# Optimization experiments

Hardware: AMD Instinct MI355X
Metric: run time of the kernel (lower is better)

The kernel has to match this reference:

```python
import jax, jax.numpy as jnp
import numpy as np

N_NODES, N_EDGES, N_FEAT, N_HID = 50000, 800000, 512, 64


def gcn_conv(x, W, b, src, dst, ew):
    """PyG-style GCNConv: linear -> symmetric-normalized aggregation with self-loops -> +bias."""
    N = x.shape[0]
    h = x @ W  # [N, H]
    # degree includes the implicit self-loop of weight 1 (PyG gcn_norm default)
    deg = jax.ops.segment_sum(ew, dst, num_segments=N) + 1.0
    dinv = jax.lax.rsqrt(deg)  # deg^{-1/2}
    coef = dinv[src] * ew * dinv[dst]  # [E]
    out = jax.ops.segment_sum(h[src] * coef[:, None], dst, num_segments=N)
    out = out + h * (dinv * dinv)[:, None]  # self-loop contribution
    return out + b


def setup_inputs() -> dict:
    key = jax.random.key(0)
    k0, k1, k2, k3 = jax.random.split(key, 4)
    x = jax.random.normal(k0, (N_NODES, N_FEAT), dtype=jnp.float32)
    edge_index = jax.random.randint(k1, (2, N_EDGES), 0, N_NODES, dtype=jnp.int64)
    edge_weight = jnp.ones((N_EDGES,), dtype=jnp.float32)
    W1 = jax.random.normal(k2, (N_FEAT, N_HID), dtype=jnp.float32) * (1.0 / np.sqrt(N_FEAT))
    b1 = jnp.zeros((N_HID,), dtype=jnp.float32)
    W2 = jax.random.normal(k3, (N_HID, N_HID), dtype=jnp.float32) * (1.0 / np.sqrt(N_HID))
    b2 = jnp.zeros((N_HID,), dtype=jnp.float32)
    return {"x": x, "edge_index": edge_index, "edge_weight": edge_weight,
            "W1": W1, "b1": b1, "W2": W2, "b2": b2}


def reference(x, edge_index, edge_weight, W1, b1, W2, b2):
    # Grace.forward -> GCN_body.forward in eval mode (no dropout, no LN)
    src, dst = edge_index[0], edge_index[1]
    h = jax.nn.relu(gcn_conv(x, W1, b1, src, dst, edge_weight))
    h = jax.nn.relu(gcn_conv(h, W2, b2, src, dst, edge_weight))
    return h
```

## Files before the change

kernel.cpp:

```cpp
#include <hip/hip_runtime.h>
#include <hip/hip_bf16.h>

typedef __bf16 bf16x8 __attribute__((ext_vector_type(8)));
typedef float  f32x4  __attribute__((ext_vector_type(4)));

#define RNODES 64
#define ROWCAP 1792
#define NB 256
#define MAXNR 1024
#define FIXB 256

__device__ __forceinline__ float bf_lo(unsigned int v) { return __uint_as_float(v << 16); }
__device__ __forceinline__ float bf_hi(unsigned int v) { return __uint_as_float(v & 0xFFFF0000u); }

__device__ __forceinline__ void pack_one(const void* __restrict__ W, int f16,
                                         __hip_bfloat16* __restrict__ Wp, int K, int t) {
    int j  = t & 7;
    int l  = (t >> 3) & 63;
    int nt = (t >> 9) & 3;
    int kt = t >> 11;
    int k = kt * 32 + (l >> 4) * 8 + j;
    int n = nt * 16 + (l & 15);
    size_t gi = (size_t)k * 64 + n;
    Wp[t] = f16 ? ((const __hip_bfloat16*)W)[gi]
                : __float2bfloat16(((const float*)W)[gi]);
}

__global__ void setup_kernel(const unsigned int* __restrict__ ew_raw,
                             const unsigned int* __restrict__ ei_raw,
                             const void* __restrict__ W1, const void* __restrict__ W2,
                             int* __restrict__ flags,
                             __hip_bfloat16* __restrict__ W1p, __hip_bfloat16* __restrict__ W2p,
                             int F, int H) {
    int f16 = (ew_raw[0] == 0x3F803F80u) ? 1 : 0;
    if (blockIdx.x == 0 && threadIdx.x == 0) {
        flags[0] = f16;
        flags[1] = ((ei_raw[1] | ei_raw[3] | ei_raw[5] | ei_raw[7]) == 0u) ? 1 : 0;
        flags[2] = 0;
        flags[3] = 0;
        flags[4] = 1;
    }
    int t = blockIdx.x * 256 + threadIdx.x;
    if (t < F * 64)            pack_one(W1, f16, W1p, F, t);
    else if (t < (F + H) * 64) pack_one(W2, f16, W2p, H, t - F * 64);
}

__device__ __forceinline__ void gemm_body(const void* __restrict__ A,
                                          const __hip_bfloat16* __restrict__ Wp,
                                          int a_f32, __hip_bfloat16* __restrict__ out,
                                          int M, int K, int gt) {
    int wid  = gt >> 6;
    int lane = gt & 63;
    if (wid >= (M >> 4)) return;
    int row0 = wid << 4;
    int quad = lane >> 4, mr = lane & 15;

    const bf16x8* bp = (const bf16x8*)((const void*)Wp) + lane;

    f32x4 acc[4];
    #pragma unroll
    for (int nt = 0; nt < 4; ++nt) acc[nt] = (f32x4){0.f, 0.f, 0.f, 0.f};

    int KT = K >> 5;
    const __hip_bfloat16* ab   = (const __hip_bfloat16*)A + (size_t)(row0 + mr) * K + quad * 8;
    const float*          af32 = (const float*)A + (size_t)(row0 + mr) * K + quad * 8;

    int kt = 0;
    for (; kt + 4 <= KT; kt += 4) {
        bf16x8 af[4];
        if (a_f32) {
            #pragma unroll
            for (int u = 0; u < 4; ++u) {
                const float* ar = af32 + (kt + u) * 32;
                #pragma unroll
                for (int j = 0; j < 8; ++j) af[u][j] = (__bf16)ar[j];
            }
        } else {
            #pragma unroll
            for (int u = 0; u < 4; ++u)
                af[u] = ((const bf16x8*)((const void*)(ab + (kt + u) * 32)))[0];
        }
        #pragma unroll
        for (int u = 0; u < 4; ++u)
            #pragma unroll
            for (int nt = 0; nt < 4; ++nt) {
                bf16x8 bf = bp[((kt + u) * 4 + nt) * 64];
                acc[nt] = __builtin_amdgcn_mfma_f32_16x16x32_bf16(af[u], bf, acc[nt], 0, 0, 0);
            }
    }
    for (; kt < KT; ++kt) {
        bf16x8 af;
        if (a_f32) {
            const float* ar = af32 + kt * 32;
            #pragma unroll
            for (int j = 0; j < 8; ++j) af[j] = (__bf16)ar[j];
        } else {
            af = ((const bf16x8*)((const void*)(ab + kt * 32)))[0];
        }
        #pragma unroll
        for (int nt = 0; nt < 4; ++nt) {
            bf16x8 bf = bp[(kt * 4 + nt) * 64];
            acc[nt] = __builtin_amdgcn_mfma_f32_16x16x32_bf16(af, bf, acc[nt], 0, 0, 0);
        }
    }

    __hip_bfloat16* o = out + (size_t)row0 * 64;
    #pragma unroll
    for (int nt = 0; nt < 4; ++nt)
        #pragma unroll
        for (int r = 0; r < 4; ++r)
            o[(size_t)(quad * 4 + r) * 64 + nt * 16 + mr] = __float2bfloat16(acc[nt][r]);
}

__global__ void gemm_mfma(const void* __restrict__ A, const __hip_bfloat16* __restrict__ Wp,
                          const int* __restrict__ flags, __hip_bfloat16* __restrict__ out,
                          int M, int K, int a_mode) {
    int gt = blockIdx.x * blockDim.x + threadIdx.x;
    int a_f32 = (a_mode == 2) && (flags[0] == 0);
    gemm_body(A, Wp, a_f32, out, M, K, gt);
}

__global__ void bgp1_kernel(const void* __restrict__ A, const __hip_bfloat16* __restrict__ Wp,
                            __hip_bfloat16* __restrict__ outH,
                            const int* __restrict__ ei, const void* __restrict__ ew,
                            int* __restrict__ flags,
                            int* __restrict__ blockhist, unsigned int* __restrict__ pkstage,
                            int M, int K, int E, int NR, int gblocks) {
    if ((int)blockIdx.x < gblocks) {
        int gt = blockIdx.x * 256 + threadIdx.x;
        gemm_body(A, Wp, flags[0] == 0, outH, M, K, gt);
        return;
    }
    __shared__ int hist[MAXNR];
    int b = blockIdx.x - gblocks, tid = threadIdx.x;
    for (int i = tid; i < NR; i += 256) hist[i] = 0;
    __syncthreads();
    int f16 = flags[0], i64 = flags[1];

    int nw = f16 ? (E >> 1) : E;
    unsigned int expect = f16 ? 0x3F803F80u : 0x3F800000u;
    int wchunk = (nw + NB - 1) / NB;
    int w0 = b * wchunk, w1 = w0 + wchunk; if (w1 > nw) w1 = nw;
    const unsigned int* ewr = (const unsigned int*)ew;
    unsigned int bad = 0;
    for (int i = w0 + tid; i < w1; i += 256) bad |= (ewr[i] ^ expect);
    if (bad) flags[4] = 0;

    int chunk = (E + NB - 1) / NB;
    int e0 = b * chunk, e1 = e0 + chunk; if (e1 > E) e1 = E;
    for (int e = e0 + tid; e < e1; e += 256) {
        int s, d;
        if (i64) { s = ei[2LL * e]; d = ei[2LL * ((long long)E + e)]; }
        else     { s = ei[e];       d = ei[E + e]; }
        int r = d >> 6;
        atomicAdd(&hist[r], 1);
        pkstage[e] = ((unsigned int)r << 22) | ((unsigned int)s << 6) | (unsigned int)(d & 63);
    }
    __syncthreads();
    for (int i = tid; i < NR; i += 256) blockhist[b * NR + i] = hist[i];
}

__device__ __forceinline__ void check_body(const void* __restrict__ A, const void* __restrict__ W,
                                           int* __restrict__ flags,
                                           const __hip_bfloat16* __restrict__ out,
                                           int N, int K, int a_mode, int fidx, int bid) {
    __shared__ float xs[4 * 512];
    int f16 = flags[0];
    int a_f32 = (a_mode == 2) && (f16 == 0);
    int tid = threadIdx.x;
    int total = 4 * K;
    for (int t = tid; t < total; t += 256) {
        int nn = t / K, kk = t - nn * K;
        int n = (int)(((long long)(bid * 4 + nn) * 977) % N);
        long long gi = (long long)n * K + kk;
        float v = a_f32 ? (float)(__bf16)(((const float*)A)[gi])
                        : __bfloat162float(((const __hip_bfloat16*)A)[gi]);
        xs[t] = v;
    }
    __syncthreads();
    int j = tid & 63, local = tid >> 6;
    int n = (int)(((long long)(bid * 4 + local) * 977) % N);
    const float* xr = xs + local * K;
    float acc = 0.f;
    if (f16) {
        const __hip_bfloat16* Wb = (const __hip_bfloat16*)W;
        #pragma unroll 8
        for (int k = 0; k < K; ++k) acc += xr[k] * __bfloat162float(Wb[(long long)k * 64 + j]);
    } else {
        const float* Wf = (const float*)W;
        #pragma unroll 8
        for (int k = 0; k < K; ++k) acc += xr[k] * (float)(__bf16)(Wf[(long long)k * 64 + j]);
    }
    float d = __bfloat162float(out[(size_t)n * 64 + j]) - acc;
    if (!(fabsf(d) <= 0.05f)) atomicAdd(&flags[fidx], 1);
}

__device__ __forceinline__ void fix_body(const void* __restrict__ A, const void* __restrict__ W,
                                         const int* __restrict__ flags,
                                         __hip_bfloat16* __restrict__ out,
                                         int N, int K, int a_mode, int fidx,
                                         int bid, int nblocks) {
    if (flags[fidx] == 0) return;
    __shared__ float xs[4 * 512];
    int tid = threadIdx.x;
    int f16 = flags[0];
    int a_f32 = (a_mode == 2) && (f16 == 0);
    int total = 4 * K;
    for (int node0 = bid * 4; node0 < N; node0 += nblocks * 4) {
        __syncthreads();
        for (int t = tid; t < total; t += 256) {
            int nn = t / K, kk = t - nn * K;
            if (node0 + nn < N) {
                long long gi = (long long)(node0 + nn) * K + kk;
                xs[t] = a_f32 ? ((const float*)A)[gi]
                              : __bfloat162float(((const __hip_bfloat16*)A)[gi]);
            }
        }
        __syncthreads();
        int j = tid & 63, local = tid >> 6;
        int n = node0 + local;
        if (n < N) {
            const float* xr = xs + local * K;
            float acc = 0.f;
            if (f16) {
                const __hip_bfloat16* Wb = (const __hip_bfloat16*)W;
                #pragma unroll 8
                for (int k = 0; k < K; ++k) acc += xr[k] * __bfloat162float(Wb[(long long)k * 64 + j]);
            } else {
                const float* Wf = (const float*)W;
                #pragma unroll 8
                for (int k = 0; k < K; ++k) acc += xr[k] * Wf[(long long)k * 64 + j];
            }
            out[(long long)n * 64 + j] = __float2bfloat16(acc);
        }
    }
}

__global__ void p2chk_kernel(int* __restrict__ blockhist, int* __restrict__ rtot, int NR,
                             const void* __restrict__ A, const void* __restrict__ W,
                             int* __restrict__ flags, const __hip_bfloat16* __restrict__ out,
                             int N, int K, int a_mode, int fidx, int p2b) {
    if ((int)blockIdx.x < p2b) {
        int r = blockIdx.x * 256 + threadIdx.x;
        if (r >= NR) return;
        int run = r * ROWCAP;
        #pragma unroll 4
        for (int b = 0; b < NB; ++b) {
            int c = blockhist[b * NR + r];
            blockhist[b * NR + r] = run;
            run += c;
        }
        int tot = run - r * ROWCAP;
        rtot[r] = tot > ROWCAP ? ROWCAP : tot;
    } else {
        check_body(A, W, flags, out, N, K, a_mode, fidx, blockIdx.x - p2b);
    }
}

__global__ void p3fix_kernel(const int* __restrict__ blockhist,
                             const unsigned int* __restrict__ pkstage,
                             const void* __restrict__ ew, const int* __restrict__ flags,
                             unsigned int* __restrict__ sortedR, float* __restrict__ sortedRW,
                             int E, int NR,
                             const void* __restrict__ A, const void* __restrict__ W,
                             __hip_bfloat16* __restrict__ out,
                             int N, int K, int a_mode, int fidx) {
    if ((int)blockIdx.x < NB) {
        __shared__ int loff[MAXNR];
        int b = blockIdx.x, tid = threadIdx.x;
        for (int i = tid; i < NR; i += 256) loff[i] = blockhist[b * NR + i];
        __syncthreads();
        int chunk = (E + NB - 1) / NB;
        int e0 = b * chunk, e1 = e0 + chunk; if (e1 > E) e1 = E;
        int ones = flags[4], f16 = flags[0];
        for (int e = e0 + tid; e < e1; e += 256) {
            unsigned int pk = pkstage[e];
            int r = (int)(pk >> 22);
            int pos = atomicAdd(&loff[r], 1);
            if (pos < (r + 1) * ROWCAP) {
                sortedR[pos] = pk;
                if (!ones) {
                    float w = f16 ? __bfloat162float(((const __hip_bfloat16*)ew)[e])
                                  : ((const float*)ew)[e];
                    sortedRW[pos] = w;
                }
            }
        }
    } else {
        fix_body(A, W, flags, out, N, K, a_mode, fidx, blockIdx.x - NB, FIXB);
    }
}

__global__ void range_kernel(const unsigned int* __restrict__ sortedR,
                             const float* __restrict__ sortedRW,
                             const int* __restrict__ rtot, const int* __restrict__ flags,
                             int* __restrict__ cnt, float* __restrict__ dinv,
                             int* __restrict__ row_ptr,
                             int* __restrict__ sortedS, float* __restrict__ sortedW, int N) {
    __shared__ unsigned int sd[ROWCAP];
    __shared__ float sw[ROWCAP];
    __shared__ int   cnt0[RNODES], pref[RNODES], slot[RNODES];
    __shared__ float wsum[RNODES];

    int r   = blockIdx.x;
    int tid = threadIdx.x;
    int ones = flags[4];
    int T = rtot[r];

    if (tid < RNODES) { cnt0[tid] = 0; wsum[tid] = 0.f; }
    __syncthreads();

    size_t g = (size_t)r * ROWCAP;
    for (int t = tid; t < T; t += 256) {
        sd[t] = sortedR[g + t];
        if (!ones) sw[t] = sortedRW[g + t];
    }
    __syncthreads();

    for (int k = tid; k < T; k += 256) {
        int dl = sd[k] & (RNODES - 1);
        atomicAdd(&cnt0[dl], 1);
        if (!ones) atomicAdd(&wsum[dl], sw[k]);
    }
    __syncthreads();

    if (tid < RNODES) pref[tid] = cnt0[tid];
    __syncthreads();
    for (int off = 1; off < RNODES; off <<= 1) {
        int v = (tid < RNODES && tid >= off) ? pref[tid - off] : 0;
        __syncthreads();
        if (tid < RNODES) pref[tid] += v;
        __syncthreads();
    }
    if (tid < RNODES) {
        int excl = pref[tid] - cnt0[tid];
        int n = r * RNODES + tid;
        slot[tid] = r * ROWCAP + excl;
        if (n < N) {
            cnt[n]     = cnt0[tid];
            row_ptr[n] = r * ROWCAP + excl;
            float wd = ones ? (float)cnt0[tid] : wsum[tid];
            dinv[n]  = rsqrtf(wd + 1.0f);
        }
    }
    __syncthreads();

    for (int k = tid; k < T; k += 256) {
        unsigned int v = sd[k];
        int dl = v & (RNODES - 1);
        int p = atomicAdd(&slot[dl], 1);
        sortedS[p] = (int)((v >> 6) & 0xFFFFu);
        if (!ones) sortedW[p] = sw[k];
    }
}

__global__ void check_fast(const void* __restrict__ A, const void* __restrict__ W,
                           int* __restrict__ flags, const __hip_bfloat16* __restrict__ out,
                           int N, int K, int a_mode, int fidx) {
    check_body(A, W, flags, out, N, K, a_mode, fidx, blockIdx.x);
}

__global__ void gemm_fix(const void* __restrict__ A, const void* __restrict__ W,
                         const int* __restrict__ flags, __hip_bfloat16* __restrict__ out,
                         int N, int K, int a_mode, int fidx) {
    fix_body(A, W, flags, out, N, K, a_mode, fidx, blockIdx.x, FIXB);
}

__global__ void gather_kernel(const __hip_bfloat16* __restrict__ h,
                              const int* __restrict__ sortedS, const float* __restrict__ sortedW,
                              const int* __restrict__ cnt, const int* __restrict__ row_ptr,
                              const float* __restrict__ dinv,
                              const void* __restrict__ bias, const int* __restrict__ flags,
                              void* __restrict__ out, int internal, int N) {
    int gt = blockIdx.x * blockDim.x + threadIdx.x;
    int n = gt >> 5, jl = gt & 31;
    if (n >= N) return;
    int f16 = flags[0], ones = flags[4];
    float dn = dinv[n];
    int deg = cnt[n];
    int base = row_ptr[n];
    const int*   p  = sortedS + base;
    const float* pw = sortedW + base;
    const unsigned int* h32 = (const unsigned int*)h;
    float a0 = 0.f, a1 = 0.f;
    int s = 0;
    for (; s + 4 <= deg; s += 4) {
        int s0 = p[s], s1 = p[s + 1], s2 = p[s + 2], s3 = p[s + 3];
        float c0 = dinv[s0] * dn, c1 = dinv[s1] * dn;
        float c2 = dinv[s2] * dn, c3 = dinv[s3] * dn;
        if (!ones) { c0 *= pw[s]; c1 *= pw[s + 1]; c2 *= pw[s + 2]; c3 *= pw[s + 3]; }
        unsigned int v0 = h32[(size_t)s0 * 32 + jl];
        unsigned int v1 = h32[(size_t)s1 * 32 + jl];
        unsigned int v2 = h32[(size_t)s2 * 32 + jl];
        unsigned int v3 = h32[(size_t)s3 * 32 + jl];
        a0 += c0 * bf_lo(v0) + c1 * bf_lo(v1) + c2 * bf_lo(v2) + c3 * bf_lo(v3);
        a1 += c0 * bf_hi(v0) + c1 * bf_hi(v1) + c2 * bf_hi(v2) + c3 * bf_hi(v3);
    }
    for (; s < deg; ++s) {
        int s0 = p[s];
        float c = dinv[s0] * dn;
        if (!ones) c *= pw[s];
        unsigned int v = h32[(size_t)s0 * 32 + jl];
        a0 += c * bf_lo(v);
        a1 += c * bf_hi(v);
    }
    unsigned int vs = h32[(size_t)n * 32 + jl];
    float dn2 = dn * dn;
    a0 += dn2 * bf_lo(vs);
    a1 += dn2 * bf_hi(vs);
    if (f16) {
        unsigned int bv = ((const unsigned int*)bias)[jl];
        a0 += bf_lo(bv);
        a1 += bf_hi(bv);
    } else {
        a0 += ((const float*)bias)[jl * 2];
        a1 += ((const float*)bias)[jl * 2 + 1];
    }
    a0 = fmaxf(a0, 0.f);
    a1 = fmaxf(a1, 0.f);
    if (internal | f16) {
        __hip_bfloat16 b0 = __float2bfloat16(a0), b1 = __float2bfloat16(a1);
        unsigned int pack = ((unsigned int)(*(unsigned short*)&b1) << 16)
                          | (unsigned int)(*(unsigned short*)&b0);
        ((unsigned int*)out)[(size_t)n * 32 + jl] = pack;
    } else {
        ((float*)out)[(size_t)n * 64 + jl * 2]     = a0;
        ((float*)out)[(size_t)n * 64 + jl * 2 + 1] = a1;
    }
}

extern "C" void kernel_launch(void* const* d_in, const int* in_sizes, int n_in,
                              void* d_out, int out_size, void* d_ws, size_t ws_size,
                              hipStream_t stream) {
    const void* x  = d_in[0];
    const int*  ei = (const int*)d_in[1];
    const void* ew = d_in[2];
    const void* W1 = d_in[3];
    const void* b1 = d_in[4];
    const void* W2 = d_in[5];
    const void* b2 = d_in[6];

    const int H = in_sizes[4];
    const int F = in_sizes[3] / H;
    const int N = in_sizes[0] / F;
    const int E = in_sizes[1] / 2;

    const int NR = (N + RNODES - 1) / RNODES;

    char* w = (char*)d_ws;
    size_t off = 0;
    auto alloc = [&](size_t bytes) {
        char* r = w + off;
        off += (bytes + 255) & ~(size_t)255;
        return r;
    };
    int*   flags     = (int*)alloc(32);
    int*   blockhist = (int*)alloc((size_t)NB * NR * 4);
    int*   rtot      = (int*)alloc((size_t)NR * 4);
    int*   cnt       = (int*)alloc((size_t)N * 4);
    float* dinv      = (float*)alloc((size_t)N * 4);
    int*   row_ptr   = (int*)alloc((size_t)N * 4);
    unsigned int* pkstage = (unsigned int*)alloc((size_t)E * 4);
    unsigned int* sortedR = (unsigned int*)alloc((size_t)NR * ROWCAP * 4);
    float* sortedRW  = (float*)alloc((size_t)NR * ROWCAP * 4);
    int*   sortedS   = (int*)alloc((size_t)NR * ROWCAP * 4);
    float* sortedW   = (float*)alloc((size_t)NR * ROWCAP * 4);
    __hip_bfloat16* bufH = (__hip_bfloat16*)alloc((size_t)N * 64 * 2);
    __hip_bfloat16* bufR = (__hip_bfloat16*)alloc((size_t)N * 64 * 2);
    __hip_bfloat16* W1p  = (__hip_bfloat16*)alloc((size_t)F * 64 * 2);
    __hip_bfloat16* W2p  = (__hip_bfloat16*)alloc((size_t)H * 64 * 2);

    int gblocks = ((N / 16) * 64 + 255) / 256;
    int p2b = (NR + 255) / 256;

    setup_kernel<<<((F + H) * 64 + 255) / 256, 256, 0, stream>>>(
        (const unsigned int*)ew, (const unsigned int*)ei, W1, W2, flags, W1p, W2p, F, H);

    bgp1_kernel<<<gblocks + NB, 256, 0, stream>>>(x, W1p, bufH, ei, ew, flags,
                                                  blockhist, pkstage,
                                                  N, F, E, NR, gblocks);

    p2chk_kernel<<<p2b + 64, 256, 0, stream>>>(blockhist, rtot, NR,
                                               x, W1, flags, bufH, N, F, 2, 2, p2b);

    p3fix_kernel<<<NB + FIXB, 256, 0, stream>>>(blockhist, pkstage, ew, flags,
                                                sortedR, sortedRW, E, NR,
                                                x, W1, bufH, N, F, 2, 2);

    range_kernel<<<NR, 256, 0, stream>>>(sortedR, sortedRW, rtot, flags,
                                         cnt, dinv, row_ptr, sortedS, sortedW, N);

    gather_kernel<<<(N * 32 + 255) / 256, 256, 0, stream>>>(bufH, sortedS, sortedW,
                                                            cnt, row_ptr, dinv,
                                                            b1, flags, bufR, 1, N);
    gemm_mfma<<<gblocks, 256, 0, stream>>>(bufR, W2p, flags, bufH, N, H, 0);
    check_fast<<<64, 256, 0, stream>>>(bufR, W2, flags, bufH, N, H, 0, 3);
    gemm_fix<<<FIXB, 256, 0, stream>>>(bufR, W2, flags, bufH, N, H, 0, 3);

    gather_kernel<<<(N * 32 + 255) / 256, 256, 0, stream>>>(bufH, sortedS, sortedW,
                                                            cnt, row_ptr, dinv,
                                                            b2, flags, d_out, 0, N);
}
```

Baseline: 313.3 us.

## Halve histogram blocks, wave-parallel prefix scan, deeper GEMM K unroll

Cuts the number of edge-bucketing blocks from 256 to 128, which halves the per-row histogram scan length. The scan over those blocks becomes wave-parallel, with one 64-lane wavefront per row using shuffle-up instead of a serial loop per thread. The MFMA GEMM inner loop is unrolled over 8 K-tiles instead of 4 to issue more loads before the MFMAs. Fewer binning blocks means less parallelism in the histogram and scatter phases, and the deeper unroll raises register pressure.

```diff
diff --git a/kernel.cpp b/kernel.cpp
--- a/kernel.cpp
+++ b/kernel.cpp
@@ -6,7 +6,7 @@
 
 #define RNODES 64
 #define ROWCAP 1792
-#define NB 256
+#define NB 128
 #define MAXNR 1024
 #define FIXB 256
 
@@ -54,7 +54,6 @@
     if (wid >= (M >> 4)) return;
     int row0 = wid << 4;
     int quad = lane >> 4, mr = lane & 15;
-
     const bf16x8* bp = (const bf16x8*)((const void*)Wp) + lane;
 
     f32x4 acc[4];
@@ -62,54 +61,52 @@
     for (int nt = 0; nt < 4; ++nt) acc[nt] = (f32x4){0.f, 0.f, 0.f, 0.f};
 
     int KT = K >> 5;
-    const __hip_bfloat16* ab   = (const __hip_bfloat16*)A + (size_t)(row0 + mr) * K + quad * 8;
-    const float*          af32 = (const float*)A + (size_t)(row0 + mr) * K + quad * 8;
+    const __hip_bfloat16* ab    = (const __hip_bfloat16*)A + (size_t)(row0 + mr) * K + quad * 8;
+    const float*          af32p = (const float*)A + (size_t)(row0 + mr) * K + quad * 8;
 
     int kt = 0;
-    for (; kt + 4 <= KT; kt += 4) {
-        bf16x8 af[4];
+    for (; kt + 8 <= KT; kt += 8) {
+        bf16x8 af[8];
         if (a_f32) {
             #pragma unroll
-            for (int u = 0; u < 4; ++u) {
-                const float* ar = af32 + (kt + u) * 32;
+            for (int u = 0; u < 8; ++u) {
+                const float* ar = af32p + (kt + u) * 32;
                 #pragma unroll
                 for (int j = 0; j < 8; ++j) af[u][j] = (__bf16)ar[j];
             }
         } else {
             #pragma unroll
-            for (int u = 0; u < 4; ++u)
+            for (int u = 0; u < 8; ++u)
                 af[u] = ((const bf16x8*)((const void*)(ab + (kt + u) * 32)))[0];
         }
         #pragma unroll
-        for (int u = 0; u < 4; ++u)
+        for (int u = 0; u < 8; ++u)
             #pragma unroll
-            for (int nt = 0; nt < 4; ++nt) {
-                bf16x8 bf = bp[((kt + u) * 4 + nt) * 64];
-                acc[nt] = __builtin_amdgcn_mfma_f32_16x16x32_bf16(af[u], bf, acc[nt], 0, 0, 0);
-            }
+            for (int nt = 0; nt < 4; ++nt)
+                acc[nt] = __builtin_amdgcn_mfma_f32_16x16x32_bf16(
+                              af[u], bp[((kt + u) * 4 + nt) * 64], acc[nt], 0, 0, 0);
     }
     for (; kt < KT; ++kt) {
         bf16x8 af;
         if (a_f32) {
-            const float* ar = af32 + kt * 32;
+            const float* ar = af32p + kt * 32;
             #pragma unroll
             for (int j = 0; j < 8; ++j) af[j] = (__bf16)ar[j];
         } else {
             af = ((const bf16x8*)((const void*)(ab + kt * 32)))[0];
         }
         #pragma unroll
-        for (int nt = 0; nt < 4; ++nt) {
-            bf16x8 bf = bp[(kt * 4 + nt) * 64];
-            acc[nt] = __builtin_amdgcn_mfma_f32_16x16x32_bf16(af, bf, acc[nt], 0, 0, 0);
-        }
+        for (int nt = 0; nt < 4; ++nt)
+            acc[nt] = __builtin_amdgcn_mfma_f32_16x16x32_bf16(
+                          af, bp[(kt * 4 + nt) * 64], acc[nt], 0, 0, 0);
     }
 
     __hip_bfloat16* o = out + (size_t)row0 * 64;
     #pragma unroll
     for (int nt = 0; nt < 4; ++nt)
         #pragma unroll
-        for (int r = 0; r < 4; ++r)
-            o[(size_t)(quad * 4 + r) * 64 + nt * 16 + mr] = __float2bfloat16(acc[nt][r]);
+        for (int rr = 0; rr < 4; ++rr)
+            o[(size_t)(quad * 4 + rr) * 64 + nt * 16 + mr] = __float2bfloat16(acc[nt][rr]);
 }
 
 __global__ void gemm_mfma(const void* __restrict__ A, const __hip_bfloat16* __restrict__ Wp,
@@ -127,8 +124,7 @@
                             int* __restrict__ blockhist, unsigned int* __restrict__ pkstage,
                             int M, int K, int E, int NR, int gblocks) {
     if ((int)blockIdx.x < gblocks) {
-        int gt = blockIdx.x * 256 + threadIdx.x;
-        gemm_body(A, Wp, flags[0] == 0, outH, M, K, gt);
+        gemm_body(A, Wp, flags[0] == 0, outH, M, K, blockIdx.x * 256 + threadIdx.x);
         return;
     }
     __shared__ int hist[MAXNR];
@@ -241,17 +237,24 @@
                              int* __restrict__ flags, const __hip_bfloat16* __restrict__ out,
                              int N, int K, int a_mode, int fidx, int p2b) {
     if ((int)blockIdx.x < p2b) {
-        int r = blockIdx.x * 256 + threadIdx.x;
-        if (r >= NR) return;
-        int run = r * ROWCAP;
-        #pragma unroll 4
-        for (int b = 0; b < NB; ++b) {
-            int c = blockhist[b * NR + r];
-            blockhist[b * NR + r] = run;
-            run += c;
-        }
-        int tot = run - r * ROWCAP;
-        rtot[r] = tot > ROWCAP ? ROWCAP : tot;
+        int r    = blockIdx.x * 4 + (threadIdx.x >> 6);
+        int lane = threadIdx.x & 63;
+        if (r < NR) {
+            int b0 = lane * 2;
+            int c0 = blockhist[(size_t)b0 * NR + r];
+            int c1 = blockhist[(size_t)(b0 + 1) * NR + r];
+            int s = c0 + c1;
+            int incl = s;
+            #pragma unroll
+            for (int off = 1; off < 64; off <<= 1) {
+                int t = __shfl_up(incl, off, 64);
+                if (lane >= off) incl += t;
+            }
+            int run = r * ROWCAP + (incl - s);
+            blockhist[(size_t)b0 * NR + r]       = run;
+            blockhist[(size_t)(b0 + 1) * NR + r] = run + c0;
+            if (lane == 63) rtot[r] = incl > ROWCAP ? ROWCAP : incl;
+        }
     } else {
         check_body(A, W, flags, out, N, K, a_mode, fidx, blockIdx.x - p2b);
     }
@@ -471,7 +474,7 @@
     __hip_bfloat16* W2p  = (__hip_bfloat16*)alloc((size_t)H * 64 * 2);
 
     int gblocks = ((N / 16) * 64 + 255) / 256;
-    int p2b = (NR + 255) / 256;
+    int p2b = (NR + 3) / 4;
 
     setup_kernel<<<((F + H) * 64 + 255) / 256, 256, 0, stream>>>(
         (const unsigned int*)ew, (const unsigned int*)ei, W1, W2, flags, W1p, W2p, F, H);
```

After: 310.4 us. No clear change (-1.0%).
